# Performance work log

Hardware: AMD Instinct MI355X
Metric: run time of the kernel (lower is better)

The kernel has to match this reference:

```python
import jax, jax.numpy as jnp
import numpy as np

NPOINT = 2048

def setup_inputs() -> dict:
    key = jax.random.key(0)
    xyz = jax.random.normal(key, (32, 3, 65536), dtype=jnp.float32)
    return {"xyz": xyz}

def furthest_point_sampling(pts, npoint):
    # pts: [B, N, 3] -> indices [B, npoint] int32
    B, N, _ = pts.shape
    batch = jnp.arange(B)

    def step(carry, _):
        dist, farthest = carry  # dist [B,N], farthest [B]
        centroid = pts[batch, farthest]              # [B, 3]
        d = jnp.sum((pts - centroid[:, None, :]) ** 2, axis=-1)  # [B, N]
        dist = jnp.minimum(dist, d)
        nxt = jnp.argmax(dist, axis=-1).astype(jnp.int32)
        return (dist, nxt), farthest

    init = (jnp.full((B, N), 1e10, dtype=pts.dtype),
            jnp.zeros((B,), dtype=jnp.int32))
    _, idx = jax.lax.scan(step, init, None, length=npoint)
    return idx.T  # [B, npoint]

def reference(xyz):
    # xyz: [B, 3, N]; module permutes to [B, N, 3] and runs FPS
    pts = jnp.transpose(xyz, (0, 2, 1)).astype(jnp.float32)
    return furthest_point_sampling(pts, NPOINT)
```

## Files before the change

kernel.cpp:

```cpp
#include <hip/hip_runtime.h>
#include <stdint.h>

#pragma clang fp contract(off)

#define NPT      2048
#define NBATCH   32
#define NPTS     65536
#define MEMBERS  8
#define NTHREADS 512
#define CHUNK    (NPTS / MEMBERS)
#define PPT      (CHUNK / NTHREADS)
#define WPB      (NTHREADS / 64)
#define PADSLOTS 32

__device__ __forceinline__ uint32_t f2u(float f) { return __float_as_uint(f); }
__device__ __forceinline__ float u2f(uint32_t u) { return __uint_as_float(u); }

__device__ __forceinline__ void amerge(float& v, int& i, float ov, int oi) {
    if (ov > v || (ov == v && oi < i)) { v = ov; i = oi; }
}

template<int CTRL>
__device__ __forceinline__ void dpp_round(float& v, int& i) {
    float ov = u2f((uint32_t)__builtin_amdgcn_mov_dpp((int)f2u(v), CTRL, 0xf, 0xf, true));
    int   oi = __builtin_amdgcn_mov_dpp(i, CTRL, 0xf, 0xf, true);
    amerge(v, i, ov, oi);
}
__device__ __forceinline__ void swz16_round(float& v, int& i) {
    float ov = u2f((uint32_t)__builtin_amdgcn_ds_swizzle((int)f2u(v), 0x401F));
    int   oi = __builtin_amdgcn_ds_swizzle(i, 0x401F);
    amerge(v, i, ov, oi);
}
__device__ __forceinline__ void row16_argmax(float& v, int& i) {
    dpp_round<0xB1>(v, i);
    dpp_round<0x4E>(v, i);
    dpp_round<0x141>(v, i);
    dpp_round<0x140>(v, i);
}
__device__ __forceinline__ void oct_argmax(float& v, int& i) {
    dpp_round<0xB1>(v, i);
    dpp_round<0x4E>(v, i);
    dpp_round<0x141>(v, i);
}

__global__ void __launch_bounds__(NTHREADS)
fps_kernel(const float* __restrict__ xyz, int* __restrict__ out,
           uint64_t* __restrict__ cand)
{
    __shared__ float    sx[CHUNK];
    __shared__ uint64_t red[WPB * 4];
    __shared__ uint32_t bc[4];

    const int i = blockIdx.x;
    const int q = i >> 3;
    const int batch  = (i & 7) * 4 + (q & 3);
    const int member = q >> 2;
    const int tid  = threadIdx.x;
    const int lane = tid & 63;
    const int wv   = tid >> 6;

    const float* xb = xyz + (size_t)batch * 3 * NPTS;
    const int gbase = member * CHUNK;

    float py[PPT], pz[PPT], pd[PPT];
#pragma unroll
    for (int k = 0; k < PPT; ++k) {
        int p = tid + k * NTHREADS;
        int g = gbase + p;
        sx[p] = xb[g];
        py[k] = xb[NPTS + g];
        pz[k] = xb[2 * NPTS + g];
        pd[k] = 1e10f;
    }

    float cx = xb[0], cy = xb[NPTS], cz = xb[2 * NPTS];
    if (member == 0 && tid == 0) out[(size_t)batch * NPT] = 0;

    uint64_t* cb = cand + (size_t)batch * 2 * PADSLOTS;

    for (int t = 0; t < NPT - 1; ++t) {
        float bv = -1.0f;
        int   bi = 0;
#pragma unroll
        for (int k = 0; k < PPT; ++k) {
            int p = tid + k * NTHREADS;
            float dx = sx[p] - cx;
            float dy = py[k] - cy;
            float dz = pz[k] - cz;
            float d  = dx * dx + dy * dy;
            d = d + dz * dz;
            float nd = fminf(pd[k], d);
            pd[k] = nd;
            bool g = nd > bv;
            bv = g ? nd : bv;
            bi = g ? (gbase + p) : bi;
        }

        row16_argmax(bv, bi);
        if ((lane & 15) == 0)
            red[wv * 4 + (lane >> 4)] = ((uint64_t)f2u(bv) << 32) | (uint32_t)bi;
        __syncthreads();

        if (wv == 0) {
            uint64_t c = red[lane & 31];
            float v  = u2f((uint32_t)(c >> 32));
            int   ix = (int)(uint32_t)(c & 0xFFFFFFFFu);
            row16_argmax(v, ix);
            swz16_round(v, ix);

            uint64_t* sb = cb + (size_t)(t & 1) * PADSLOTS;
            const uint32_t tag = (uint32_t)t;
            if (lane == 0) {
                uint64_t w = ((uint64_t)f2u(v) << 32)
                           | ((uint64_t)(uint32_t)ix << 16) | tag;
                __hip_atomic_store(&sb[member], w, __ATOMIC_RELAXED,
                                   __HIP_MEMORY_SCOPE_AGENT);
            }

            uint64_t w = 0; bool done = false;
            do {
                if (!done) w = __hip_atomic_load(&sb[lane & 7], __ATOMIC_RELAXED,
                                                 __HIP_MEMORY_SCOPE_AGENT);
                done = (uint32_t)(w & 0xFFFFu) == tag;
            } while (!__all(done));

            float gv = u2f((uint32_t)(w >> 32));
            int   gi = (int)((w >> 16) & 0xFFFFu);
            oct_argmax(gv, gi);

            float wx = xb[gi], wy = xb[NPTS + gi], wz = xb[2 * NPTS + gi];
            if (lane == 0) {
                bc[0] = f2u(wx); bc[1] = f2u(wy); bc[2] = f2u(wz);
                if (member == 0) out[(size_t)batch * NPT + t + 1] = gi;
            }
        }
        __syncthreads();
        cx = u2f(bc[0]); cy = u2f(bc[1]); cz = u2f(bc[2]);
    }
}

extern "C" void kernel_launch(void* const* d_in, const int* in_sizes, int n_in,
                              void* d_out, int out_size, void* d_ws, size_t ws_size,
                              hipStream_t stream)
{
    const float* xyz = (const float*)d_in[0];
    int* out = (int*)d_out;
    uint64_t* cand = (uint64_t*)d_ws;
    fps_kernel<<<NBATCH * MEMBERS, NTHREADS, 0, stream>>>(xyz, out, cand);
}
```

Before: 4.302 ms.

## Replace block barriers with tagged LDS flags and prefetch candidate coordinates

Doubles the threads per block and removes both __syncthreads per iteration. Waves now publish tagged per-wave argmax results to double-buffered LDS slots, and the next centroid is handed over through a tag-flagged broadcast buffer. Wave 0 runs at raised priority and fetches each member's candidate coordinates while still polling, so the global load after the cross-block argmax is gone. This also stores a loop index instead of the global index in the inner loop and does a full-wave reduction. Spin-waiting in LDS risks contention and subtle ordering bugs.

Result: slower. 5.119 ms (+19.0%).

```diff
diff --git a/kernel.cpp b/kernel.cpp
--- a/kernel.cpp
+++ b/kernel.cpp
@@ -7,11 +7,11 @@
 #define NBATCH   32
 #define NPTS     65536
 #define MEMBERS  8
-#define NTHREADS 512
+#define NTHREADS 1024
 #define CHUNK    (NPTS / MEMBERS)
 #define PPT      (CHUNK / NTHREADS)
 #define WPB      (NTHREADS / 64)
-#define PADSLOTS 32
+#define LINEPAD  16
 
 __device__ __forceinline__ uint32_t f2u(float f) { return __float_as_uint(f); }
 __device__ __forceinline__ float u2f(uint32_t u) { return __uint_as_float(u); }
@@ -19,7 +19,6 @@
 __device__ __forceinline__ void amerge(float& v, int& i, float ov, int oi) {
     if (ov > v || (ov == v && oi < i)) { v = ov; i = oi; }
 }
-
 template<int CTRL>
 __device__ __forceinline__ void dpp_round(float& v, int& i) {
     float ov = u2f((uint32_t)__builtin_amdgcn_mov_dpp((int)f2u(v), CTRL, 0xf, 0xf, true));
@@ -30,6 +29,19 @@
     float ov = u2f((uint32_t)__builtin_amdgcn_ds_swizzle((int)f2u(v), 0x401F));
     int   oi = __builtin_amdgcn_ds_swizzle(i, 0x401F);
     amerge(v, i, ov, oi);
+}
+__device__ __forceinline__ void shfl32_round(float& v, int& i) {
+    float ov = __shfl_xor(v, 32, 64);
+    int   oi = __shfl_xor(i, 32, 64);
+    amerge(v, i, ov, oi);
+}
+__device__ __forceinline__ void wave_argmax(float& v, int& i) {
+    dpp_round<0xB1>(v, i);
+    dpp_round<0x4E>(v, i);
+    dpp_round<0x141>(v, i);
+    dpp_round<0x140>(v, i);
+    swz16_round(v, i);
+    shfl32_round(v, i);
 }
 __device__ __forceinline__ void row16_argmax(float& v, int& i) {
     dpp_round<0xB1>(v, i);
@@ -48,8 +60,8 @@
            uint64_t* __restrict__ cand)
 {
     __shared__ float    sx[CHUNK];
-    __shared__ uint64_t red[WPB * 4];
-    __shared__ uint32_t bc[4];
+    __shared__ uint64_t red[2][WPB];
+    __shared__ uint32_t bc[2][4];
 
     const int i = blockIdx.x;
     const int q = i >> 3;
@@ -73,14 +85,29 @@
         pd[k] = 1e10f;
     }
 
-    float cx = xb[0], cy = xb[NPTS], cz = xb[2 * NPTS];
-    if (member == 0 && tid == 0) out[(size_t)batch * NPT] = 0;
+    if (tid == 0) {
+        bc[0][0] = f2u(xb[0]); bc[0][1] = f2u(xb[NPTS]); bc[0][2] = f2u(xb[2 * NPTS]);
+        bc[0][3] = 0;
+        bc[1][3] = 0xFFFFFFFFu;
+        if (member == 0) out[(size_t)batch * NPT] = 0;
+    }
+    if (tid < 2 * WPB) red[tid >> 4][tid & 15] = ~0ull;
+    __syncthreads();
 
-    uint64_t* cb = cand + (size_t)batch * 2 * PADSLOTS;
+    uint64_t* cb = cand + (size_t)batch * 2 * LINEPAD;
+    volatile uint32_t* vbc0 = &bc[0][0];
+    volatile uint32_t* vbc1 = &bc[1][0];
 
     for (int t = 0; t < NPT - 1; ++t) {
+        const int par = t & 1;
+        const uint32_t tag = (uint32_t)t;
+        volatile uint32_t* vb = par ? vbc1 : vbc0;
+
+        while (vb[3] != tag) {}
+        float cx = u2f(vb[0]), cy = u2f(vb[1]), cz = u2f(vb[2]);
+
         float bv = -1.0f;
-        int   bi = 0;
+        int   bk = 0;
 #pragma unroll
         for (int k = 0; k < PPT; ++k) {
             int p = tid + k * NTHREADS;
@@ -92,24 +119,28 @@
             float nd = fminf(pd[k], d);
             pd[k] = nd;
             bool g = nd > bv;
-            bv = g ? nd : bv;
-            bi = g ? (gbase + p) : bi;
+            bv = fmaxf(bv, nd);
+            bk = g ? k : bk;
         }
+        int bi = gbase + tid + (bk << 10);
 
-        row16_argmax(bv, bi);
-        if ((lane & 15) == 0)
-            red[wv * 4 + (lane >> 4)] = ((uint64_t)f2u(bv) << 32) | (uint32_t)bi;
-        __syncthreads();
+        wave_argmax(bv, bi);
+        if (lane == 0)
+            ((volatile uint64_t*)&red[par][wv])[0] =
+                ((uint64_t)f2u(bv) << 32) | ((uint64_t)(uint32_t)bi << 16) | tag;
 
         if (wv == 0) {
-            uint64_t c = red[lane & 31];
+            __builtin_amdgcn_s_setprio(1);
+            uint64_t c; bool rok = false;
+            do {
+                c = ((volatile uint64_t*)&red[par][lane & 15])[0];
+                rok = (uint32_t)(c & 0xFFFFu) == tag;
+            } while (!__all(rok));
             float v  = u2f((uint32_t)(c >> 32));
-            int   ix = (int)(uint32_t)(c & 0xFFFFFFFFu);
+            int   ix = (int)((c >> 16) & 0xFFFFu);
             row16_argmax(v, ix);
-            swz16_round(v, ix);
 
-            uint64_t* sb = cb + (size_t)(t & 1) * PADSLOTS;
-            const uint32_t tag = (uint32_t)t;
+            uint64_t* sb = cb + (size_t)par * LINEPAD;
             if (lane == 0) {
                 uint64_t w = ((uint64_t)f2u(v) << 32)
                            | ((uint64_t)(uint32_t)ix << 16) | tag;
@@ -117,25 +148,43 @@
                                    __HIP_MEMORY_SCOPE_AGENT);
             }
 
-            uint64_t w = 0; bool done = false;
+            uint64_t* ap = &sb[lane & 7];
+            uint64_t w = 0; bool done = false, fetched = false;
+            float wx = 0.f, wy = 0.f, wz = 0.f; int mi = -1;
             do {
-                if (!done) w = __hip_atomic_load(&sb[lane & 7], __ATOMIC_RELAXED,
-                                                 __HIP_MEMORY_SCOPE_AGENT);
-                done = (uint32_t)(w & 0xFFFFu) == tag;
+                if (!done) {
+                    uint64_t x = __hip_atomic_load(ap, __ATOMIC_RELAXED,
+                                                   __HIP_MEMORY_SCOPE_AGENT);
+                    if ((uint32_t)(x & 0xFFFFu) == tag) { w = x; done = true; }
+                }
+                if (done && !fetched) {
+                    fetched = true;
+                    if (lane < 8) {
+                        mi = (int)((w >> 16) & 0xFFFFu);
+                        wx = xb[mi]; wy = xb[NPTS + mi]; wz = xb[2 * NPTS + mi];
+                    }
+                }
             } while (!__all(done));
 
             float gv = u2f((uint32_t)(w >> 32));
             int   gi = (int)((w >> 16) & 0xFFFFu);
             oct_argmax(gv, gi);
 
-            float wx = xb[gi], wy = xb[NPTS + gi], wz = xb[2 * NPTS + gi];
+            uint64_t mk = __ballot(mi == gi);
+            int wl = (int)(__ffsll((unsigned long long)mk) - 1);
+            float fx = __shfl(wx, wl, 64);
+            float fy = __shfl(wy, wl, 64);
+            float fz = __shfl(wz, wl, 64);
+
             if (lane == 0) {
-                bc[0] = f2u(wx); bc[1] = f2u(wy); bc[2] = f2u(wz);
                 if (member == 0) out[(size_t)batch * NPT + t + 1] = gi;
+                volatile uint32_t* nb = (par ^ 1) ? vbc1 : vbc0;
+                nb[0] = f2u(fx); nb[1] = f2u(fy); nb[2] = f2u(fz);
+                __threadfence_block();
+                nb[3] = tag + 1;
             }
+            __builtin_amdgcn_s_setprio(0);
         }
-        __syncthreads();
-        cx = u2f(bc[0]); cy = u2f(bc[1]); cz = u2f(bc[2]);
     }
 }
 
```
